# Kernel tuning notes

Measured on AMD Instinct MI355X. Metric: run time of the kernel, lower is better.

Reference implementation:

```python
import jax, jax.numpy as jnp
import numpy as np

B, T, D, H, L, V, CTX = 4, 2048, 256, 8, 12, 256, 2048
HD = D // H


def _ln(x, w, b, eps=1e-5):
    m = x.mean(-1, keepdims=True)
    v = ((x - m) ** 2).mean(-1, keepdims=True)
    return (x - m) * jax.lax.rsqrt(v + eps) * w + b


def setup_inputs() -> dict:
    key = jax.random.key(0)
    ks = jax.random.split(key, 16)
    s = 0.02
    inp = {
        "x": jax.random.randint(ks[0], (B, T), 0, V, dtype=jnp.int32),
        "tok_embed": jax.random.normal(ks[1], (V, D), jnp.float32) * s,
        "pos_embed": jax.random.normal(ks[2], (CTX, D), jnp.float32) * s,
        # stacked per-layer params (leading axis = layer)
        "ln1_w": jnp.ones((L, D), jnp.float32),
        "ln1_b": jnp.zeros((L, D), jnp.float32),
        "qkv_w": jax.random.normal(ks[3], (L, D, 3 * D), jnp.float32) * s,
        "qkv_b": jnp.zeros((L, 3 * D), jnp.float32),
        "out_w": jax.random.normal(ks[4], (L, D, D), jnp.float32) * s,
        "out_b": jnp.zeros((L, D), jnp.float32),
        "ln2_w": jnp.ones((L, D), jnp.float32),
        "ln2_b": jnp.zeros((L, D), jnp.float32),
        "fc1_w": jax.random.normal(ks[5], (L, D, 4 * D), jnp.float32) * s,
        "fc1_b": jnp.zeros((L, 4 * D), jnp.float32),
        "fc2_w": jax.random.normal(ks[6], (L, 4 * D, D), jnp.float32) * s,
        "fc2_b": jnp.zeros((L, D), jnp.float32),
        "lnf_w": jnp.ones((D,), jnp.float32),
        "lnf_b": jnp.zeros((D,), jnp.float32),
        "head_w": jax.random.normal(ks[7], (D, V), jnp.float32) * s,
        "head_b": jnp.zeros((V,), jnp.float32),
    }
    return inp


def _forward(x, tok_embed, pos_embed, ln1_w, ln1_b, qkv_w, qkv_b, out_w, out_b,
             ln2_w, ln2_b, fc1_w, fc1_b, fc2_w, fc2_b, lnf_w, lnf_b, head_w, head_b):
    Tcur = x.shape[1]
    h = tok_embed[x] + pos_embed[:Tcur][None, :, :]  # (B,T,D)
    causal = jnp.triu(jnp.ones((Tcur, Tcur), bool), k=1)  # True above diagonal
    scale = jnp.sqrt(jnp.asarray(HD, h.dtype))

    def step(h, p):
        (l1w, l1b, qw, qb, ow, ob, l2w, l2b, f1w, f1b, f2w, f2b) = p
        # attention
        z = _ln(h, l1w, l1b)
        qkv = z @ qw + qb  # (B,T,3D)
        qkv = qkv.reshape(h.shape[0], Tcur, 3, H, HD)
        q, k, v = qkv[:, :, 0], qkv[:, :, 1], qkv[:, :, 2]  # (B,T,H,HD)
        attn = jnp.einsum('bqhd,bkhd->bhqk', q, k) / scale
        attn = jnp.where(causal, -jnp.inf, attn)
        attn = jax.nn.softmax(attn, axis=-1)
        o = jnp.einsum('bhqk,bkhd->bqhd', attn, v).reshape(h.shape[0], Tcur, D)
        h = h + o @ ow + ob
        # MLP (torch nn.GELU default = exact erf gelu)
        z = _ln(h, l2w, l2b)
        z = jax.nn.gelu(z @ f1w + f1b, approximate=False)
        h = h + z @ f2w + f2b
        return h, None

    params = (ln1_w, ln1_b, qkv_w, qkv_b, out_w, out_b,
              ln2_w, ln2_b, fc1_w, fc1_b, fc2_w, fc2_b)
    h, _ = jax.lax.scan(step, h, params)
    h = _ln(h, lnf_w, lnf_b)
    return h @ head_w + head_b  # (B,T,V)


def reference(x, tok_embed, pos_embed, ln1_w, ln1_b, qkv_w, qkv_b, out_w, out_b,
              ln2_w, ln2_b, fc1_w, fc1_b, fc2_w, fc2_b, lnf_w, lnf_b, head_w, head_b):
    return _forward(x, tok_embed, pos_embed, ln1_w, ln1_b, qkv_w, qkv_b, out_w, out_b,
                    ln2_w, ln2_b, fc1_w, fc1_b, fc2_w, fc2_b, lnf_w, lnf_b, head_w, head_b)
```

## Files before the change

### kernel.cpp

```cpp
#include <hip/hip_runtime.h>
#include <cstdint>

#define TT 2048
#define DD 256
#define HH 8
#define LL 12

typedef __attribute__((ext_vector_type(8))) short s16x8;
typedef __attribute__((ext_vector_type(4))) float f32x4;

__device__ __forceinline__ unsigned short f2bf(float f) {
  union { float f; unsigned u; } v; v.f = f;
  return (unsigned short)((v.u + 0x7FFFu + ((v.u >> 16) & 1u)) >> 16);
}

__device__ __forceinline__ unsigned cvtpk(float lo, float hi) {
  unsigned r;
  asm("v_cvt_pk_bf16_f32 %0, %1, %2" : "=v"(r) : "v"(lo), "v"(hi));
  return r;
}

__device__ __forceinline__ float geluf(float x) {
  return 0.5f * x * (1.0f + erff(x * 0.70710678118654752f));
}

__device__ __forceinline__ float fexp2(float x) {
  float r;
  asm("v_exp_f32 %0, %1" : "=v"(r) : "v"(x));
  return r;
}

__device__ __forceinline__ void gload16(const void* g, void* l) {
  __builtin_amdgcn_global_load_lds((const __attribute__((address_space(1))) unsigned int*)g,
                                   (__attribute__((address_space(3))) unsigned int*)l, 16, 0, 0);
}

__global__ __launch_bounds__(256) void k_embed(const int* __restrict__ x,
                                               const float* __restrict__ tok,
                                               const float* __restrict__ pos,
                                               float* __restrict__ h) {
  int i = blockIdx.x * 256 + threadIdx.x;
  int row = i >> 6, c = i & 63;
  int t = x[row];
  f32x4 tv = ((const f32x4*)(tok + (size_t)t * DD))[c];
  f32x4 pv = ((const f32x4*)(pos + (size_t)(row & (TT - 1)) * DD))[c];
  ((f32x4*)(h + (size_t)row * DD))[c] = tv + pv;
}

__global__ __launch_bounds__(256) void k_ln(const float* __restrict__ h,
                                            const float* __restrict__ wgt,
                                            const float* __restrict__ bia,
                                            unsigned short* __restrict__ z) {
  int row = blockIdx.x * 4 + (threadIdx.x >> 6);
  int lane = threadIdx.x & 63;
  f32x4 v = ((const f32x4*)(h + (size_t)row * DD))[lane];
  float s = v[0] + v[1] + v[2] + v[3];
#pragma unroll
  for (int m = 32; m; m >>= 1) s += __shfl_xor(s, m);
  float mean = s * (1.0f / DD);
  f32x4 d = v - mean;
  float s2 = d[0] * d[0] + d[1] * d[1] + d[2] * d[2] + d[3] * d[3];
#pragma unroll
  for (int m = 32; m; m >>= 1) s2 += __shfl_xor(s2, m);
  float inv = rsqrtf(s2 * (1.0f / DD) + 1e-5f);
  f32x4 wv = ((const f32x4*)wgt)[lane];
  f32x4 bv = ((const f32x4*)bia)[lane];
  float o0 = d[0] * inv * wv[0] + bv[0], o1 = d[1] * inv * wv[1] + bv[1];
  float o2 = d[2] * inv * wv[2] + bv[2], o3 = d[3] * inv * wv[3] + bv[3];
  unsigned long long u64 = (unsigned long long)cvtpk(o0, o1) |
                           ((unsigned long long)cvtpk(o2, o3) << 32);
  *(unsigned long long*)(z + (size_t)row * DD + lane * 4) = u64;
}

__global__ __launch_bounds__(256) void k_cast_all(const float* __restrict__ qw, const float* __restrict__ ow,
                                                  const float* __restrict__ f1, const float* __restrict__ f2,
                                                  unsigned short* __restrict__ dst) {
  __shared__ float Tt[32][33];
  const int l = blockIdx.y;
  const int t = blockIdx.x;
  const float* src;
  unsigned short* d;
  int K, N, tk, tn;
  if (t < 192) {
    src = qw + (size_t)l * 196608; d = dst + (size_t)l * 786432;
    K = 256; N = 768; tk = t / 24; tn = t % 24;
  } else if (t < 256) {
    int t2 = t - 192;
    src = ow + (size_t)l * 65536; d = dst + (size_t)l * 786432 + 196608;
    K = 256; N = 256; tk = t2 >> 3; tn = t2 & 7;
  } else if (t < 512) {
    int t3 = t - 256;
    src = f1 + (size_t)l * 262144; d = dst + (size_t)l * 786432 + 262144;
    K = 256; N = 1024; tk = t3 >> 5; tn = t3 & 31;
  } else {
    int t4 = t - 512;
    src = f2 + (size_t)l * 262144; d = dst + (size_t)l * 786432 + 524288;
    K = 1024; N = 256; tk = t4 >> 3; tn = t4 & 7;
  }
  const int tx = threadIdx.x & 31, ty = threadIdx.x >> 5;
#pragma unroll
  for (int r = 0; r < 4; ++r) {
    int row = ty + r * 8;
    Tt[row][tx] = src[(size_t)(tk * 32 + row) * N + tn * 32 + tx];
  }
  __syncthreads();
#pragma unroll
  for (int r = 0; r < 4; ++r) {
    int row = ty + r * 8;
    d[(size_t)(tn * 32 + row) * K + tk * 32 + tx] = f2bf(Tt[tx][row]);
  }
}

__global__ __launch_bounds__(256) void k_cast_tr4(const float* __restrict__ qw, const float* __restrict__ ow,
                                                  const float* __restrict__ f1, const float* __restrict__ f2,
                                                  unsigned short* __restrict__ dq, unsigned short* __restrict__ dO,
                                                  unsigned short* __restrict__ d1, unsigned short* __restrict__ d2) {
// ... 66 lines not shown
      for (int ni = 0; ni < 4; ++ni)
        bf[ni] = *(const s16x8*)(Bs[buf] + (wc * 64 + ni * 16 + l15) * 64 + ks * 32 + g * 8);
#pragma unroll
      for (int mi = 0; mi < MI; ++mi)
#pragma unroll
        for (int ni = 0; ni < 4; ++ni)
          acc[mi][ni] = __builtin_amdgcn_mfma_f32_16x16x32_bf16(af[mi], bf[ni], acc[mi][ni], 0, 0, 0);
    }
    if (have_next) {
      __syncthreads();
      buf ^= 1;
    }
  }
#pragma unroll
  for (int ni = 0; ni < 4; ++ni) {
    int col = tn * 128 + wc * 64 + ni * 16 + l15;
    float bv = bias[col];
#pragma unroll
    for (int mi = 0; mi < MI; ++mi) {
      int row0 = tm * BM + wr * MI * 16 + mi * 16 + g * 4;
#pragma unroll
      for (int r = 0; r < 4; ++r) {
        size_t idx = (size_t)(row0 + r) * N + col;
        float vvv = acc[mi][ni][r] + bv;
        if (MODE == 0) ((unsigned short*)out)[idx] = f2bf(vvv);
        else if (MODE == 1) ((unsigned short*)out)[idx] = f2bf(geluf(vvv));
        else ((float*)out)[idx] = vvv;
      }
    }
  }
}

template <int NK>
__global__ __launch_bounds__(256, 2) void k_gemm_ln(const unsigned short* __restrict__ A,
                                                    const unsigned short* __restrict__ BT,
                                                    const float* __restrict__ bias,
                                                    float* __restrict__ h,
                                                    const float* __restrict__ lnw,
                                                    const float* __restrict__ lnb,
                                                    unsigned short* __restrict__ z) {
  __shared__ __align__(16) unsigned short As[2][32 * 64];
  __shared__ __align__(16) unsigned short Bs[2][256 * 64];
  const int tid = threadIdx.x;
  const int lane = tid & 63, wc = tid >> 6;
  const int l15 = lane & 15, g = lane >> 4;
  const int tm = blockIdx.x;
  const int K = NK * 64;
  f32x4 acc[2][4] = {};
  const unsigned short* Ag0 = A + (size_t)tm * 32 * K;

  gload16(Ag0 + (size_t)(tid >> 3) * K + (tid & 7) * 8, As[0] + tid * 8);
#pragma unroll
  for (int it = 0; it < 8; ++it) {
    int c = it * 256 + tid;
    gload16(BT + (size_t)(c >> 3) * K + (c & 7) * 8, Bs[0] + c * 8);
  }
  __syncthreads();

  int buf = 0;
  for (int kt = 0; kt < NK; ++kt) {
    const bool have_next = (kt + 1 < NK);
    if (have_next) {
      gload16(Ag0 + (size_t)(tid >> 3) * K + (kt + 1) * 64 + (tid & 7) * 8, As[buf ^ 1] + tid * 8);
#pragma unroll
      for (int it = 0; it < 8; ++it) {
        int c = it * 256 + tid;
        gload16(BT + (size_t)(c >> 3) * K + (kt + 1) * 64 + (c & 7) * 8, Bs[buf ^ 1] + c * 8);
      }
    }
#pragma unroll
    for (int ks = 0; ks < 2; ++ks) {
      s16x8 af[2], bf[4];
#pragma unroll
      for (int mi = 0; mi < 2; ++mi)
        af[mi] = *(const s16x8*)(As[buf] + (mi * 16 + l15) * 64 + ks * 32 + g * 8);
#pragma unroll
      for (int ni = 0; ni < 4; ++ni)
        bf[ni] = *(const s16x8*)(Bs[buf] + (wc * 64 + ni * 16 + l15) * 64 + ks * 32 + g * 8);
#pragma unroll
      for (int mi = 0; mi < 2; ++mi)
#pragma unroll
        for (int ni = 0; ni < 4; ++ni)
          acc[mi][ni] = __builtin_amdgcn_mfma_f32_16x16x32_bf16(af[mi], bf[ni], acc[mi][ni], 0, 0, 0);
    }
    if (have_next) {
      __syncthreads();
      buf ^= 1;
    }
  }
  const int row0 = tm * 32;
  float hv[2][4][4];
  float psum[2][4] = {}, psq[2][4] = {};
#pragma unroll
  for (int mi = 0; mi < 2; ++mi)
#pragma unroll
    for (int ni = 0; ni < 4; ++ni) {
      int col = wc * 64 + ni * 16 + l15;
      float bv = bias[col];
#pragma unroll
      for (int r = 0; r < 4; ++r) {
        int row = row0 + mi * 16 + g * 4 + r;
        float v = acc[mi][ni][r] + bv + h[(size_t)row * DD + col];
        hv[mi][ni][r] = v;
        h[(size_t)row * DD + col] = v;
        psum[mi][r] += v;
        psq[mi][r] += v * v;
      }
    }
#pragma unroll
  for (int m = 1; m < 16; m <<= 1)
#pragma unroll
    for (int mi = 0; mi < 2; ++mi)
#pragma unroll
      for (int r = 0; r < 4; ++r) {
        psum[mi][r] += __shfl_xor(psum[mi][r], m);
        psq[mi][r] += __shfl_xor(psq[mi][r], m);
      }
  __syncthreads();
  float* red = (float*)&As[0][0];
  if (l15 == 0) {
#pragma unroll
    for (int mi = 0; mi < 2; ++mi)
#pragma unroll
      for (int r = 0; r < 4; ++r) {
        int rw = mi * 16 + g * 4 + r;
        red[wc * 32 + rw] = psum[mi][r];
        red[128 + wc * 32 + rw] = psq[mi][r];
      }
  }
  __syncthreads();
  float mean[2][4], inv[2][4];
#pragma unroll
  for (int mi = 0; mi < 2; ++mi)
#pragma unroll
    for (int r = 0; r < 4; ++r) {
      int rw = mi * 16 + g * 4 + r;
      float s = (red[rw] + red[32 + rw]) + (red[64 + rw] + red[96 + rw]);
      float q = (red[128 + rw] + red[160 + rw]) + (red[192 + rw] + red[224 + rw]);
      float mn = s * (1.0f / DD);
      mean[mi][r] = mn;
      inv[mi][r] = rsqrtf(q * (1.0f / DD) - mn * mn + 1e-5f);
    }
#pragma unroll
  for (int ni = 0; ni < 4; ++ni) {
    int col = wc * 64 + ni * 16 + l15;
    float wv = lnw[col], bv = lnb[col];
#pragma unroll
    for (int mi = 0; mi < 2; ++mi)
#pragma unroll
      for (int r = 0; r < 4; ++r) {
        int row = row0 + mi * 16 + g * 4 + r;
        z[(size_t)row * DD + col] = f2bf((hv[mi][ni][r] - mean[mi][r]) * inv[mi][r] * wv + bv);
      }
  }
}

__global__ __launch_bounds__(512, 4) void k_attn(const unsigned short* __restrict__ qkv,
                                                 unsigned short* __restrict__ o) {
  __shared__ __align__(16) unsigned short Ks[2][128 * 40];
  __shared__ __align__(16) unsigned short Vs[2][2 * 32 * 72];
  const int tid = threadIdx.x, lane = tid & 63, wvi = tid >> 6;
  const int w = wvi >> 1, kh = wvi & 1;
  const int l15 = lane & 15, g = lane >> 4;
  const int p = blockIdx.x;
  const int b = blockIdx.y >> 3, hh = blockIdx.y & 7;
  const size_t base = (size_t)b * TT * 768 + hh * 32;
  const float scl2 = 0.25503492f;
  const int qt0 = p, qt1 = 31 - p;
  const int nt0 = (qt0 >> 1) + 1;
  const int krow = (wvi & 3) * 32 + (lane >> 1);
  const int khK = lane & 1;
  const int iv = wvi & 3;
  const int khv = iv >> 1, dh = iv & 1;

  s16x8 qf0 = *(const s16x8*)(qkv + base + (size_t)(qt0 * 64 + w * 16 + l15) * 768 + g * 8);
  s16x8 qf1 = *(const s16x8*)(qkv + base + (size_t)(qt1 * 64 + w * 16 + l15) * 768 + g * 8);

  if (wvi < 4) {
    const unsigned short* kp = qkv + base + (size_t)krow * 768 + 256 + khK * 16;
    s16x8 k0 = *(const s16x8*)kp;
    s16x8 k1 = *(const s16x8*)(kp + 8);
    *(s16x8*)(Ks[0] + krow * 40 + khK * 16) = k0;
    *(s16x8*)(Ks[0] + krow * 40 + khK * 16 + 8) = k1;
  } else {
    const unsigned short* vp = qkv + base + (size_t)(khv * 64 + lane) * 768 + 512 + dh * 16;
    s16x8 v0 = *(const s16x8*)vp;
    s16x8 v1 = *(const s16x8*)(vp + 8);
    unsigned short* vb = Vs[0] + khv * 2304;
#pragma unroll
    for (int e = 0; e < 8; ++e) {
      int d0 = dh * 16 + e, d1 = dh * 16 + 8 + e;
      vb[d0 * 72 + (lane ^ (((d0 >> 3) & 3) << 4))] = (unsigned short)v0[e];
      vb[d1 * 72 + (lane ^ (((d1 >> 3) & 3) << 4))] = (unsigned short)v1[e];
    }
  }
  __syncthreads();

  f32x4 accO[2] = {};
  float mM = -3.0e38f, ls = 0.f;

  for (int t = 0; t < 17; ++t) {
    const int buf = t & 1;
    const bool ph = (t >= nt0);
    const int qt = ph ? qt1 : qt0;
    const int j = ph ? t - nt0 : t;
    const bool have_next = (t + 1 < 17);
    unsigned short* ps = (wvi < 4) ? (Ks[buf ^ 1] + wvi * 1280)
                                   : (Vs[buf ^ 1] + (wvi - 4) * 1152);
    s16x8 k0n, k1n, v0n, v1n;
    if (have_next) {
      const int jn = (t + 1 >= nt0) ? t + 1 - nt0 : t + 1;
      if (wvi < 4) {
        const unsigned short* kp = qkv + base + (size_t)(jn * 128 + krow) * 768 + 256 + khK * 16;
        k0n = *(const s16x8*)kp;
        k1n = *(const s16x8*)(kp + 8);
      } else {
        const unsigned short* vp = qkv + base + (size_t)(jn * 128 + khv * 64 + lane) * 768 + 512 + dh * 16;
        v0n = *(const s16x8*)vp;
        v1n = *(const s16x8*)(vp + 8);
      }
    }
    const int rel = qt * 64 + w * 16 - j * 128;
    int cbg = (rel + 15) >> 4; if (cbg > 7) cbg = 7;
    const int cbm = (cbg - kh * 4 > 3) ? 3 : cbg - kh * 4;
    if (cbm >= 0) {
      const bool fullw = (rel >= kh * 64 + 63);
      f32x4 st[4];
#pragma unroll
      for (int c = 0; c < 4; ++c)
        if (c <= cbm) {
          s16x8 kf = *(const s16x8*)(Ks[buf] + (kh * 64 + c * 16 + l15) * 40 + g * 8);
          f32x4 zz = {};
          st[c] = __builtin_amdgcn_mfma_f32_16x16x32_bf16(kf, ph ? qf1 : qf0, zz, 0, 0, 0);
        }
      float rmax = -3.0e38f;
#pragma unroll
      for (int c = 0; c < 4; ++c)
        if (c <= cbm) {
          if (!fullw) {
#pragma unroll
            for (int r = 0; r < 4; ++r)
              if ((kh * 64 + c * 16 + g * 4 + r) > rel + l15) st[c][r] = -3.0e38f;
          }
#pragma unroll
          for (int r = 0; r < 4; ++r) rmax = fmaxf(rmax, st[c][r]);
        }
      rmax = fmaxf(rmax, __shfl_xor(rmax, 16));
      rmax = fmaxf(rmax, __shfl_xor(rmax, 32));
      const float rs = rmax * scl2;
      float al = 1.0f;
      if (!__all(rs <= mM + 11.5f)) {
        float nm = fmaxf(mM, rs);
        al = fexp2(mM - nm);
        mM = nm;
#pragma unroll
        for (int r = 0; r < 4; ++r) {
          float aw = __shfl(al, g * 4 + r);
          accO[0][r] *= aw;
          accO[1][r] *= aw;
        }
      }
      float rsum = 0.f;
#pragma unroll
      for (int c = 0; c < 4; ++c)
        if (c <= cbm) {
          float e0 = fexp2(fmaf(st[c][0], scl2, -mM));
          float e1 = fexp2(fmaf(st[c][1], scl2, -mM));
          float e2 = fexp2(fmaf(st[c][2], scl2, -mM));
          float e3 = fexp2(fmaf(st[c][3], scl2, -mM));
          rsum += (e0 + e1) + (e2 + e3);
          unsigned long long u = (unsigned long long)cvtpk(e0, e1) |
                                 ((unsigned long long)cvtpk(e2, e3) << 32);
          *(unsigned long long*)(ps + l15 * 72 + c * 16 + g * 4) = u;
        }
      if (cbm < 3 && !(cbm & 1))
        *(unsigned long long*)(ps + l15 * 72 + (cbm + 1) * 16 + g * 4) = 0ULL;
      rsum += __shfl_xor(rsum, 16);
      rsum += __shfl_xor(rsum, 32);
      ls = ls * al + rsum;
      asm volatile("s_waitcnt lgkmcnt(0)" ::: "memory");
      __builtin_amdgcn_sched_barrier(0);
      const int kcm = cbm >> 1;
#pragma unroll
      for (int kc = 0; kc < 2; ++kc)
        if (kc <= kcm) {
          s16x8 pa = *(const s16x8*)(ps + l15 * 72 + kc * 32 + g * 8);
          s16x8 bv0, bv1;
#pragma unroll
          for (int hb = 0; hb < 2; ++hb) {
            const int d = hb * 16 + l15;
            const int kx = (kc * 32 + g * 8) ^ (((d >> 3) & 3) << 4);
            if (hb == 0) bv0 = *(const s16x8*)(Vs[buf] + kh * 2304 + d * 72 + kx);
            else bv1 = *(const s16x8*)(Vs[buf] + kh * 2304 + d * 72 + kx);
          }
          accO[0] = __builtin_amdgcn_mfma_f32_16x16x32_bf16(pa, bv0, accO[0], 0, 0, 0);
          accO[1] = __builtin_amdgcn_mfma_f32_16x16x32_bf16(pa, bv1, accO[1], 0, 0, 0);
        }
    }
    if (have_next) {
      if (wvi < 4) {
        *(s16x8*)(Ks[buf ^ 1] + krow * 40 + khK * 16) = k0n;
        *(s16x8*)(Ks[buf ^ 1] + krow * 40 + khK * 16 + 8) = k1n;
      } else {
        unsigned short* vb = Vs[buf ^ 1] + khv * 2304;
#pragma unroll
        for (int e = 0; e < 8; ++e) {
          int d0 = dh * 16 + e, d1 = dh * 16 + 8 + e;
          vb[d0 * 72 + (lane ^ (((d0 >> 3) & 3) << 4))] = (unsigned short)v0n[e];
          vb[d1 * 72 + (lane ^ (((d1 >> 3) & 3) << 4))] = (unsigned short)v1n[e];
        }
      }
      __syncthreads();
    }
    if (t == nt0 - 1) {
      float* sc = (float*)((wvi < 4) ? (Ks[buf] + wvi * 1280) : (Vs[buf] + (wvi - 4) * 1152));
#pragma unroll
      for (int hb = 0; hb < 2; ++hb)
#pragma unroll
        for (int r = 0; r < 4; ++r) sc[(g * 4 + r) * 32 + hb * 16 + l15] = accO[hb][r];
      if (g == 0) { sc[512 + l15] = mM; sc[528 + l15] = ls; }
      __syncthreads();
      if (kh == 0) {
        const int pw = wvi + 1;
        float* pb = (float*)((pw < 4) ? (Ks[buf] + pw * 1280) : (Vs[buf] + (pw - 4) * 1152));
#pragma unroll
        for (int r = 0; r < 4; ++r) {
          int q = g * 4 + r;
          float mA = __shfl(mM, q), lA = __shfl(ls, q);
          float mB = pb[512 + q], lB = pb[528 + q];
          float M = fmaxf(mA, mB);
          float eA = fexp2(mA - M), eB = fexp2(mB - M);
          float inv = 1.0f / (eA * lA + eB * lB);
          int row = qt0 * 64 + w * 16 + q;
#pragma unroll
          for (int hb = 0; hb < 2; ++hb) {
            float ob = pb[q * 32 + hb * 16 + l15];
            float val = (eA * accO[hb][r] + eB * ob) * inv;
            o[(size_t)(b * TT + row) * DD + hh * 32 + hb * 16 + l15] = f2bf(val);
          }
        }
      }
      __syncthreads();
      accO[0] = f32x4{};
      accO[1] = f32x4{};
      mM = -3.0e38f;
      ls = 0.f;
    }
  }
  {
    __syncthreads();
    float* sc = (float*)((wvi < 4) ? (Ks[0] + wvi * 1280) : (Vs[0] + (wvi - 4) * 1152));
#pragma unroll
    for (int hb = 0; hb < 2; ++hb)
#pragma unroll
      for (int r = 0; r < 4; ++r) sc[(g * 4 + r) * 32 + hb * 16 + l15] = accO[hb][r];
    if (g == 0) { sc[512 + l15] = mM; sc[528 + l15] = ls; }
    __syncthreads();
    if (kh == 0) {
      const int pw = wvi + 1;
      float* pb = (float*)((pw < 4) ? (Ks[0] + pw * 1280) : (Vs[0] + (pw - 4) * 1152));
#pragma unroll
      for (int r = 0; r < 4; ++r) {
        int q = g * 4 + r;
        float mA = __shfl(mM, q), lA = __shfl(ls, q);
        float mB = pb[512 + q], lB = pb[528 + q];
        float M = fmaxf(mA, mB);
        float eA = fexp2(mA - M), eB = fexp2(mB - M);
        float inv = 1.0f / (eA * lA + eB * lB);
        int row = qt1 * 64 + w * 16 + q;
#pragma unroll
        for (int hb = 0; hb < 2; ++hb) {
          float ob = pb[q * 32 + hb * 16 + l15];
          float val = (eA * accO[hb][r] + eB * ob) * inv;
          o[(size_t)(b * TT + row) * DD + hh * 32 + hb * 16 + l15] = f2bf(val);
        }
      }
    }
  }
}

extern "C" void kernel_launch(void* const* d_in, const int* in_sizes, int n_in,
                              void* d_out, int out_size, void* d_ws, size_t ws_size,
                              hipStream_t stream) {
  const int* x = (const int*)d_in[0];
  const float* tok = (const float*)d_in[1];
  const float* pos = (const float*)d_in[2];
  const float* ln1w = (const float*)d_in[3];
  const float* ln1b = (const float*)d_in[4];
  const float* qkvw = (const float*)d_in[5];
  const float* qkvb = (const float*)d_in[6];
  const float* outw = (const float*)d_in[7];
  const float* outb = (const float*)d_in[8];
  const float* ln2w = (const float*)d_in[9];
  const float* ln2b = (const float*)d_in[10];
  const float* f1w = (const float*)d_in[11];
  const float* f1b = (const float*)d_in[12];
  const float* f2w = (const float*)d_in[13];
  const float* f2b = (const float*)d_in[14];
  const float* lnfw = (const float*)d_in[15];
  const float* lnfb = (const float*)d_in[16];
  const float* hw = (const float*)d_in[17];
  const float* hb = (const float*)d_in[18];

  char* ws = (char*)d_ws;
  float* h = (float*)(ws + 0);
  unsigned short* z = (unsigned short*)(ws + 8388608);
  unsigned short* qkvB = (unsigned short*)(ws + 12582912);
  unsigned short* ob = (unsigned short*)(ws + 25165824);
  unsigned short* a1 = (unsigned short*)(ws + 29360128);
  unsigned short* wAll = (unsigned short*)(ws + 46137344);
  const bool bigws = ws_size >= 65142784ULL;
  unsigned short* wh = (unsigned short*)(ws + (bigws ? 65011712 : 47710208));

  if (bigws)
    k_cast_all<<<dim3(768, 12), dim3(256), 0, stream>>>(qkvw, outw, f1w, f2w, wAll);
  k_cast_tr256<<<dim3(256), dim3(256), 0, stream>>>(hw, wh);
  k_embed<<<dim3(2048), dim3(256), 0, stream>>>(x, tok, pos, h);
  k_ln<<<dim3(2048), dim3(256), 0, stream>>>(h, ln1w, ln1b, z);

  for (int l = 0; l < LL; ++l) {
    unsigned short* wq = wAll + (size_t)(bigws ? l : 0) * 786432;
    unsigned short* wo = wq + 196608;
    unsigned short* w1 = wo + 65536;
    unsigned short* w2 = w1 + 262144;
    if (!bigws)
      k_cast_tr4<<<dim3(1024), dim3(256), 0, stream>>>(
          qkvw + (size_t)l * 196608, outw + (size_t)l * 65536,
          f1w + (size_t)l * 262144, f2w + (size_t)l * 262144, wq, wo, w1, w2);
    k_gemm<0, 2><<<dim3(6, 128), dim3(256), 0, stream>>>(z, wq, qkvb + l * 768, qkvB, nullptr, 8192, 768, 256);
    k_attn<<<dim3(16, 32), dim3(512), 0, stream>>>(qkvB, ob);
    k_gemm_ln<4><<<dim3(256), dim3(256), 0, stream>>>(ob, wo, outb + l * 256, h,
                                                      ln2w + l * 256, ln2b + l * 256, z);
    k_gemm<1, 2><<<dim3(8, 128), dim3(256), 0, stream>>>(z, w1, f1b + l * 1024, a1, nullptr, 8192, 1024, 256);
    const float* nw = (l == LL - 1) ? lnfw : ln1w + (l + 1) * 256;
    const float* nb = (l == LL - 1) ? lnfb : ln1b + (l + 1) * 256;
    k_gemm_ln<16><<<dim3(256), dim3(256), 0, stream>>>(a1, w2, f2b + l * 256, h, nw, nb, z);
  }

  k_gemm<3, 2><<<dim3(2, 128), dim3(256), 0, stream>>>(z, wh, hb, d_out, nullptr, 8192, 256, 256);
}
```

Before: 1.288 ms.

## Split attention key tile four ways across waves and halve query tile size

The attention kernel now uses 32-row query tiles, paired as p and 63-p, and launches twice as many blocks. Each wave handles a 16-query slice against a quarter (32 keys) of each 128-key tile instead of a half. The four partial softmax states are merged at the end through shared memory, and launch bounds are raised to target more resident blocks. The aim is more parallelism and shorter per-wave dependency chains, paid for with extra merge work, more redundant K/V tile loads per query, and more register pressure.

```diff
diff --git a/kernel.cpp b/kernel.cpp
--- a/kernel.cpp
+++ b/kernel.cpp
@@ -337,26 +337,26 @@
   }
 }
 
-__global__ __launch_bounds__(512, 4) void k_attn(const unsigned short* __restrict__ qkv,
+__global__ __launch_bounds__(512, 8) void k_attn(const unsigned short* __restrict__ qkv,
                                                  unsigned short* __restrict__ o) {
   __shared__ __align__(16) unsigned short Ks[2][128 * 40];
   __shared__ __align__(16) unsigned short Vs[2][2 * 32 * 72];
   const int tid = threadIdx.x, lane = tid & 63, wvi = tid >> 6;
-  const int w = wvi >> 1, kh = wvi & 1;
+  const int w = wvi >> 2, kq = wvi & 3;
   const int l15 = lane & 15, g = lane >> 4;
   const int p = blockIdx.x;
   const int b = blockIdx.y >> 3, hh = blockIdx.y & 7;
   const size_t base = (size_t)b * TT * 768 + hh * 32;
   const float scl2 = 0.25503492f;
-  const int qt0 = p, qt1 = 31 - p;
-  const int nt0 = (qt0 >> 1) + 1;
+  const int qt0 = p, qt1 = 63 - p;
+  const int nt0 = (qt0 >> 2) + 1;
   const int krow = (wvi & 3) * 32 + (lane >> 1);
   const int khK = lane & 1;
   const int iv = wvi & 3;
   const int khv = iv >> 1, dh = iv & 1;
 
-  s16x8 qf0 = *(const s16x8*)(qkv + base + (size_t)(qt0 * 64 + w * 16 + l15) * 768 + g * 8);
-  s16x8 qf1 = *(const s16x8*)(qkv + base + (size_t)(qt1 * 64 + w * 16 + l15) * 768 + g * 8);
+  s16x8 qf0 = *(const s16x8*)(qkv + base + (size_t)(qt0 * 32 + w * 16 + l15) * 768 + g * 8);
+  s16x8 qf1 = *(const s16x8*)(qkv + base + (size_t)(qt1 * 32 + w * 16 + l15) * 768 + g * 8);
 
   if (wvi < 4) {
     const unsigned short* kp = qkv + base + (size_t)krow * 768 + 256 + khK * 16;
@@ -402,27 +402,27 @@
         v1n = *(const s16x8*)(vp + 8);
       }
     }
-    const int rel = qt * 64 + w * 16 - j * 128;
+    const int rel = qt * 32 + w * 16 - j * 128;
     int cbg = (rel + 15) >> 4; if (cbg > 7) cbg = 7;
-    const int cbm = (cbg - kh * 4 > 3) ? 3 : cbg - kh * 4;
+    const int cbm = (cbg - kq * 2 > 1) ? 1 : cbg - kq * 2;
     if (cbm >= 0) {
-      const bool fullw = (rel >= kh * 64 + 63);
-      f32x4 st[4];
-#pragma unroll
-      for (int c = 0; c < 4; ++c)
+      const bool fullw = (rel >= kq * 32 + 31);
+      f32x4 st[2];
+#pragma unroll
+      for (int c = 0; c < 2; ++c)
         if (c <= cbm) {
-          s16x8 kf = *(const s16x8*)(Ks[buf] + (kh * 64 + c * 16 + l15) * 40 + g * 8);
+          s16x8 kf = *(const s16x8*)(Ks[buf] + (kq * 32 + c * 16 + l15) * 40 + g * 8);
           f32x4 zz = {};
           st[c] = __builtin_amdgcn_mfma_f32_16x16x32_bf16(kf, ph ? qf1 : qf0, zz, 0, 0, 0);
         }
       float rmax = -3.0e38f;
 #pragma unroll
-      for (int c = 0; c < 4; ++c)
+      for (int c = 0; c < 2; ++c)
         if (c <= cbm) {
           if (!fullw) {
 #pragma unroll
             for (int r = 0; r < 4; ++r)
-              if ((kh * 64 + c * 16 + g * 4 + r) > rel + l15) st[c][r] = -3.0e38f;
+              if ((kq * 32 + c * 16 + g * 4 + r) > rel + l15) st[c][r] = -3.0e38f;
           }
 #pragma unroll
           for (int r = 0; r < 4; ++r) rmax = fmaxf(rmax, st[c][r]);
@@ -444,7 +444,7 @@
       }
       float rsum = 0.f;
 #pragma unroll
-      for (int c = 0; c < 4; ++c)
+      for (int c = 0; c < 2; ++c)
         if (c <= cbm) {
           float e0 = fexp2(fmaf(st[c][0], scl2, -mM));
           float e1 = fexp2(fmaf(st[c][1], scl2, -mM));
@@ -453,31 +453,28 @@
           rsum += (e0 + e1) + (e2 + e3);
           unsigned long long u = (unsigned long long)cvtpk(e0, e1) |
                                  ((unsigned long long)cvtpk(e2, e3) << 32);
-          *(unsigned long long*)(ps + l15 * 72 + c * 16 + g * 4) = u;
-        }
-      if (cbm < 3 && !(cbm & 1))
-        *(unsigned long long*)(ps + l15 * 72 + (cbm + 1) * 16 + g * 4) = 0ULL;
+          *(unsigned long long*)(ps + l15 * 40 + c * 16 + g * 4) = u;
+        }
+      if (cbm < 1)
+        *(unsigned long long*)(ps + l15 * 40 + 16 + g * 4) = 0ULL;
       rsum += __shfl_xor(rsum, 16);
       rsum += __shfl_xor(rsum, 32);
       ls = ls * al + rsum;
       asm volatile("s_waitcnt lgkmcnt(0)" ::: "memory");
       __builtin_amdgcn_sched_barrier(0);
-      const int kcm = cbm >> 1;
-#pragma unroll
-      for (int kc = 0; kc < 2; ++kc)
-        if (kc <= kcm) {
-          s16x8 pa = *(const s16x8*)(ps + l15 * 72 + kc * 32 + g * 8);
-          s16x8 bv0, bv1;
-#pragma unroll
-          for (int hb = 0; hb < 2; ++hb) {
-            const int d = hb * 16 + l15;
-            const int kx = (kc * 32 + g * 8) ^ (((d >> 3) & 3) << 4);
-            if (hb == 0) bv0 = *(const s16x8*)(Vs[buf] + kh * 2304 + d * 72 + kx);
-            else bv1 = *(const s16x8*)(Vs[buf] + kh * 2304 + d * 72 + kx);
-          }
-          accO[0] = __builtin_amdgcn_mfma_f32_16x16x32_bf16(pa, bv0, accO[0], 0, 0, 0);
-          accO[1] = __builtin_amdgcn_mfma_f32_16x16x32_bf16(pa, bv1, accO[1], 0, 0, 0);
-        }
+      {
+        s16x8 pa = *(const s16x8*)(ps + l15 * 40 + g * 8);
+        s16x8 bv0, bv1;
+#pragma unroll
+        for (int hb = 0; hb < 2; ++hb) {
+          const int d = hb * 16 + l15;
+          const int kx = ((kq & 1) * 32 + g * 8) ^ (((d >> 3) & 3) << 4);
+          if (hb == 0) bv0 = *(const s16x8*)(Vs[buf] + (kq >> 1) * 2304 + d * 72 + kx);
+          else bv1 = *(const s16x8*)(Vs[buf] + (kq >> 1) * 2304 + d * 72 + kx);
+        }
+        accO[0] = __builtin_amdgcn_mfma_f32_16x16x32_bf16(pa, bv0, accO[0], 0, 0, 0);
+        accO[1] = __builtin_amdgcn_mfma_f32_16x16x32_bf16(pa, bv1, accO[1], 0, 0, 0);
+      }
     }
     if (have_next) {
       if (wvi < 4) {
@@ -502,23 +499,26 @@
         for (int r = 0; r < 4; ++r) sc[(g * 4 + r) * 32 + hb * 16 + l15] = accO[hb][r];
       if (g == 0) { sc[512 + l15] = mM; sc[528 + l15] = ls; }
       __syncthreads();
-      if (kh == 0) {
-        const int pw = wvi + 1;
-        float* pb = (float*)((pw < 4) ? (Ks[buf] + pw * 1280) : (Vs[buf] + (pw - 4) * 1152));
+      if (kq == 0) {
+        const float* pb1 = (const float*)((wvi + 1 < 4) ? (Ks[buf] + (wvi + 1) * 1280) : (Vs[buf] + (wvi - 3) * 1152));
+        const float* pb2 = (const float*)((wvi + 2 < 4) ? (Ks[buf] + (wvi + 2) * 1280) : (Vs[buf] + (wvi - 2) * 1152));
+        const float* pb3 = (const float*)((wvi + 3 < 4) ? (Ks[buf] + (wvi + 3) * 1280) : (Vs[buf] + (wvi - 1) * 1152));
 #pragma unroll
         for (int r = 0; r < 4; ++r) {
           int q = g * 4 + r;
-          float mA = __shfl(mM, q), lA = __shfl(ls, q);
-          float mB = pb[512 + q], lB = pb[528 + q];
-          float M = fmaxf(mA, mB);
-          float eA = fexp2(mA - M), eB = fexp2(mB - M);
-          float inv = 1.0f / (eA * lA + eB * lB);
-          int row = qt0 * 64 + w * 16 + q;
+          float m0 = __shfl(mM, q), l0 = __shfl(ls, q);
+          float m1 = pb1[512 + q], l1 = pb1[528 + q];
+          float m2 = pb2[512 + q], l2 = pb2[528 + q];
+          float m3 = pb3[512 + q], l3 = pb3[528 + q];
+          float M = fmaxf(fmaxf(m0, m1), fmaxf(m2, m3));
+          float e0 = fexp2(m0 - M), e1 = fexp2(m1 - M), e2 = fexp2(m2 - M), e3 = fexp2(m3 - M);
+          float inv = 1.0f / (e0 * l0 + e1 * l1 + e2 * l2 + e3 * l3);
+          int row = qt0 * 32 + w * 16 + q;
 #pragma unroll
           for (int hb = 0; hb < 2; ++hb) {
-            float ob = pb[q * 32 + hb * 16 + l15];
-            float val = (eA * accO[hb][r] + eB * ob) * inv;
-            o[(size_t)(b * TT + row) * DD + hh * 32 + hb * 16 + l15] = f2bf(val);
+            int oi = q * 32 + hb * 16 + l15;
+            float val = e0 * accO[hb][r] + e1 * pb1[oi] + e2 * pb2[oi] + e3 * pb3[oi];
+            o[(size_t)(b * TT + row) * DD + hh * 32 + hb * 16 + l15] = f2bf(val * inv);
           }
         }
       }
@@ -538,23 +538,26 @@
       for (int r = 0; r < 4; ++r) sc[(g * 4 + r) * 32 + hb * 16 + l15] = accO[hb][r];
     if (g == 0) { sc[512 + l15] = mM; sc[528 + l15] = ls; }
     __syncthreads();
-    if (kh == 0) {
-      const int pw = wvi + 1;
-      float* pb = (float*)((pw < 4) ? (Ks[0] + pw * 1280) : (Vs[0] + (pw - 4) * 1152));
+    if (kq == 0) {
+      const float* pb1 = (const float*)((wvi + 1 < 4) ? (Ks[0] + (wvi + 1) * 1280) : (Vs[0] + (wvi - 3) * 1152));
+      const float* pb2 = (const float*)((wvi + 2 < 4) ? (Ks[0] + (wvi + 2) * 1280) : (Vs[0] + (wvi - 2) * 1152));
+      const float* pb3 = (const float*)((wvi + 3 < 4) ? (Ks[0] + (wvi + 3) * 1280) : (Vs[0] + (wvi - 1) * 1152));
 #pragma unroll
       for (int r = 0; r < 4; ++r) {
         int q = g * 4 + r;
-        float mA = __shfl(mM, q), lA = __shfl(ls, q);
-        float mB = pb[512 + q], lB = pb[528 + q];
-        float M = fmaxf(mA, mB);
-        float eA = fexp2(mA - M), eB = fexp2(mB - M);
-        float inv = 1.0f / (eA * lA + eB * lB);
-        int row = qt1 * 64 + w * 16 + q;
+        float m0 = __shfl(mM, q), l0 = __shfl(ls, q);
+        float m1 = pb1[512 + q], l1 = pb1[528 + q];
+        float m2 = pb2[512 + q], l2 = pb2[528 + q];
+        float m3 = pb3[512 + q], l3 = pb3[528 + q];
+        float M = fmaxf(fmaxf(m0, m1), fmaxf(m2, m3));
+        float e0 = fexp2(m0 - M), e1 = fexp2(m1 - M), e2 = fexp2(m2 - M), e3 = fexp2(m3 - M);
+        float inv = 1.0f / (e0 * l0 + e1 * l1 + e2 * l2 + e3 * l3);
+        int row = qt1 * 32 + w * 16 + q;
 #pragma unroll
         for (int hb = 0; hb < 2; ++hb) {
-          float ob = pb[q * 32 + hb * 16 + l15];
-          float val = (eA * accO[hb][r] + eB * ob) * inv;
-          o[(size_t)(b * TT + row) * DD + hh * 32 + hb * 16 + l15] = f2bf(val);
+          int oi = q * 32 + hb * 16 + l15;
+          float val = e0 * accO[hb][r] + e1 * pb1[oi] + e2 * pb2[oi] + e3 * pb3[oi];
+          o[(size_t)(b * TT + row) * DD + hh * 32 + hb * 16 + l15] = f2bf(val * inv);
         }
       }
     }
@@ -610,7 +613,7 @@
           qkvw + (size_t)l * 196608, outw + (size_t)l * 65536,
           f1w + (size_t)l * 262144, f2w + (size_t)l * 262144, wq, wo, w1, w2);
     k_gemm<0, 2><<<dim3(6, 128), dim3(256), 0, stream>>>(z, wq, qkvb + l * 768, qkvB, nullptr, 8192, 768, 256);
-    k_attn<<<dim3(16, 32), dim3(512), 0, stream>>>(qkvB, ob);
+    k_attn<<<dim3(32, 32), dim3(512), 0, stream>>>(qkvB, ob);
     k_gemm_ln<4><<<dim3(256), dim3(256), 0, stream>>>(ob, wo, outb + l * 256, h,
                                                       ln2w + l * 256, ln2b + l * 256, z);
     k_gemm<1, 2><<<dim3(8, 128), dim3(256), 0, stream>>>(z, w1, f1b + l * 1024, a1, nullptr, 8192, 1024, 256);
```

Result: slower. 4.135 ms (+221.2%).

## Fuse embed with first layernorm, fold head cast, widen gemm_ln to 8 waves

Applied to the files above, without the earlier changes.

Merges the embedding gather and the first layernorm into one kernel and folds the head-weight cast into the batched weight-cast launch, removing launches and an extra pass over h. The fused GEMM+residual+layernorm kernel now uses 512 threads, so each of 8 waves computes 32 output columns. The residual read is prefetched before the K loop. This is meant to raise occupancy and latency hiding for the 256-block grid, at the cost of a larger cross-wave reduction and a shared reduction buffer that must be twice as large.

```diff
diff --git a/kernel.cpp b/kernel.cpp
--- a/kernel.cpp
+++ b/kernel.cpp
@@ -35,25 +35,20 @@
                                    (__attribute__((address_space(3))) unsigned int*)l, 16, 0, 0);
 }
 
-__global__ __launch_bounds__(256) void k_embed(const int* __restrict__ x,
-                                               const float* __restrict__ tok,
-                                               const float* __restrict__ pos,
-                                               float* __restrict__ h) {
-  int i = blockIdx.x * 256 + threadIdx.x;
-  int row = i >> 6, c = i & 63;
-  int t = x[row];
-  f32x4 tv = ((const f32x4*)(tok + (size_t)t * DD))[c];
-  f32x4 pv = ((const f32x4*)(pos + (size_t)(row & (TT - 1)) * DD))[c];
-  ((f32x4*)(h + (size_t)row * DD))[c] = tv + pv;
-}
-
-__global__ __launch_bounds__(256) void k_ln(const float* __restrict__ h,
-                                            const float* __restrict__ wgt,
-                                            const float* __restrict__ bia,
-                                            unsigned short* __restrict__ z) {
+__global__ __launch_bounds__(256) void k_embed_ln(const int* __restrict__ x,
+                                                  const float* __restrict__ tok,
+                                                  const float* __restrict__ pos,
+                                                  const float* __restrict__ wgt,
+                                                  const float* __restrict__ bia,
+                                                  float* __restrict__ h,
+                                                  unsigned short* __restrict__ z) {
   int row = blockIdx.x * 4 + (threadIdx.x >> 6);
   int lane = threadIdx.x & 63;
-  f32x4 v = ((const f32x4*)(h + (size_t)row * DD))[lane];
+  int t = x[row];
+  f32x4 tv = ((const f32x4*)(tok + (size_t)t * DD))[lane];
+  f32x4 pv = ((const f32x4*)(pos + (size_t)(row & (TT - 1)) * DD))[lane];
+  f32x4 v = tv + pv;
+  ((f32x4*)(h + (size_t)row * DD))[lane] = v;
   float s = v[0] + v[1] + v[2] + v[3];
 #pragma unroll
   for (int m = 32; m; m >>= 1) s += __shfl_xor(s, m);
@@ -74,6 +69,7 @@
 
 __global__ __launch_bounds__(256) void k_cast_all(const float* __restrict__ qw, const float* __restrict__ ow,
                                                   const float* __restrict__ f1, const float* __restrict__ f2,
+                                                  const float* __restrict__ hw,
                                                   unsigned short* __restrict__ dst) {
   __shared__ float Tt[32][33];
   const int l = blockIdx.y;
@@ -81,7 +77,11 @@
   const float* src;
   unsigned short* d;
   int K, N, tk, tn;
-  if (t < 192) {
+  if (l == 12) {
+    if (t >= 64) return;
+    src = hw; d = dst + (size_t)12 * 786432;
+    K = 256; N = 256; tk = t >> 3; tn = t & 7;
+  } else if (t < 192) {
     src = qw + (size_t)l * 196608; d = dst + (size_t)l * 786432;
     K = 256; N = 768; tk = t / 24; tn = t % 24;
   } else if (t < 256) {
@@ -214,7 +214,7 @@
 }
 
 template <int NK>
-__global__ __launch_bounds__(256, 2) void k_gemm_ln(const unsigned short* __restrict__ A,
+__global__ __launch_bounds__(512, 2) void k_gemm_ln(const unsigned short* __restrict__ A,
                                                     const unsigned short* __restrict__ BT,
                                                     const float* __restrict__ bias,
                                                     float* __restrict__ h,
@@ -228,13 +228,25 @@
   const int l15 = lane & 15, g = lane >> 4;
   const int tm = blockIdx.x;
   const int K = NK * 64;
-  f32x4 acc[2][4] = {};
+  const int row0 = tm * 32;
+  f32x4 acc[2][2] = {};
   const unsigned short* Ag0 = A + (size_t)tm * 32 * K;
 
-  gload16(Ag0 + (size_t)(tid >> 3) * K + (tid & 7) * 8, As[0] + tid * 8);
-#pragma unroll
-  for (int it = 0; it < 8; ++it) {
-    int c = it * 256 + tid;
+  float rv[2][2][4];
+#pragma unroll
+  for (int mi = 0; mi < 2; ++mi)
+#pragma unroll
+    for (int ni = 0; ni < 2; ++ni) {
+      int col = wc * 32 + ni * 16 + l15;
+#pragma unroll
+      for (int r = 0; r < 4; ++r)
+        rv[mi][ni][r] = h[(size_t)(row0 + mi * 16 + g * 4 + r) * DD + col];
+    }
+
+  if (tid < 256) gload16(Ag0 + (size_t)(tid >> 3) * K + (tid & 7) * 8, As[0] + tid * 8);
+#pragma unroll
+  for (int it = 0; it < 4; ++it) {
+    int c = it * 512 + tid;
     gload16(BT + (size_t)(c >> 3) * K + (c & 7) * 8, Bs[0] + c * 8);
   }
   __syncthreads();
@@ -243,26 +255,27 @@
   for (int kt = 0; kt < NK; ++kt) {
     const bool have_next = (kt + 1 < NK);
     if (have_next) {
-      gload16(Ag0 + (size_t)(tid >> 3) * K + (kt + 1) * 64 + (tid & 7) * 8, As[buf ^ 1] + tid * 8);
-#pragma unroll
-      for (int it = 0; it < 8; ++it) {
-        int c = it * 256 + tid;
+      if (tid < 256)
+        gload16(Ag0 + (size_t)(tid >> 3) * K + (kt + 1) * 64 + (tid & 7) * 8, As[buf ^ 1] + tid * 8);
+#pragma unroll
+      for (int it = 0; it < 4; ++it) {
+        int c = it * 512 + tid;
         gload16(BT + (size_t)(c >> 3) * K + (kt + 1) * 64 + (c & 7) * 8, Bs[buf ^ 1] + c * 8);
       }
     }
 #pragma unroll
     for (int ks = 0; ks < 2; ++ks) {
-      s16x8 af[2], bf[4];
+      s16x8 af[2], bf[2];
 #pragma unroll
       for (int mi = 0; mi < 2; ++mi)
         af[mi] = *(const s16x8*)(As[buf] + (mi * 16 + l15) * 64 + ks * 32 + g * 8);
 #pragma unroll
-      for (int ni = 0; ni < 4; ++ni)
-        bf[ni] = *(const s16x8*)(Bs[buf] + (wc * 64 + ni * 16 + l15) * 64 + ks * 32 + g * 8);
+      for (int ni = 0; ni < 2; ++ni)
+        bf[ni] = *(const s16x8*)(Bs[buf] + (wc * 32 + ni * 16 + l15) * 64 + ks * 32 + g * 8);
 #pragma unroll
       for (int mi = 0; mi < 2; ++mi)
 #pragma unroll
-        for (int ni = 0; ni < 4; ++ni)
+        for (int ni = 0; ni < 2; ++ni)
           acc[mi][ni] = __builtin_amdgcn_mfma_f32_16x16x32_bf16(af[mi], bf[ni], acc[mi][ni], 0, 0, 0);
     }
     if (have_next) {
@@ -270,19 +283,18 @@
       buf ^= 1;
     }
   }
-  const int row0 = tm * 32;
-  float hv[2][4][4];
+  float hv[2][2][4];
   float psum[2][4] = {}, psq[2][4] = {};
 #pragma unroll
   for (int mi = 0; mi < 2; ++mi)
 #pragma unroll
-    for (int ni = 0; ni < 4; ++ni) {
-      int col = wc * 64 + ni * 16 + l15;
+    for (int ni = 0; ni < 2; ++ni) {
+      int col = wc * 32 + ni * 16 + l15;
       float bv = bias[col];
 #pragma unroll
       for (int r = 0; r < 4; ++r) {
         int row = row0 + mi * 16 + g * 4 + r;
-        float v = acc[mi][ni][r] + bv + h[(size_t)row * DD + col];
+        float v = acc[mi][ni][r] + bv + rv[mi][ni][r];
         hv[mi][ni][r] = v;
         h[(size_t)row * DD + col] = v;
         psum[mi][r] += v;
@@ -307,7 +319,7 @@
       for (int r = 0; r < 4; ++r) {
         int rw = mi * 16 + g * 4 + r;
         red[wc * 32 + rw] = psum[mi][r];
-        red[128 + wc * 32 + rw] = psq[mi][r];
+        red[256 + wc * 32 + rw] = psq[mi][r];
       }
   }
   __syncthreads();
@@ -317,22 +329,26 @@
 #pragma unroll
     for (int r = 0; r < 4; ++r) {
       int rw = mi * 16 + g * 4 + r;
-      float s = (red[rw] + red[32 + rw]) + (red[64 + rw] + red[96 + rw]);
-      float q = (red[128 + rw] + red[160 + rw]) + (red[192 + rw] + red[224 + rw]);
+      float s = 0.f, q = 0.f;
+#pragma unroll
+      for (int wv = 0; wv < 8; ++wv) {
+        s += red[wv * 32 + rw];
+        q += red[256 + wv * 32 + rw];
+      }
       float mn = s * (1.0f / DD);
       mean[mi][r] = mn;
       inv[mi][r] = rsqrtf(q * (1.0f / DD) - mn * mn + 1e-5f);
     }
 #pragma unroll
-  for (int ni = 0; ni < 4; ++ni) {
-    int col = wc * 64 + ni * 16 + l15;
-    float wv = lnw[col], bv = lnb[col];
+  for (int ni = 0; ni < 2; ++ni) {
+    int col = wc * 32 + ni * 16 + l15;
+    float wvv = lnw[col], bvv = lnb[col];
 #pragma unroll
     for (int mi = 0; mi < 2; ++mi)
 #pragma unroll
       for (int r = 0; r < 4; ++r) {
         int row = row0 + mi * 16 + g * 4 + r;
-        z[(size_t)row * DD + col] = f2bf((hv[mi][ni][r] - mean[mi][r]) * inv[mi][r] * wv + bv);
+        z[(size_t)row * DD + col] = f2bf((hv[mi][ni][r] - mean[mi][r]) * inv[mi][r] * wvv + bvv);
       }
   }
 }
@@ -595,10 +611,10 @@
   unsigned short* wh = (unsigned short*)(ws + (bigws ? 65011712 : 47710208));
 
   if (bigws)
-    k_cast_all<<<dim3(768, 12), dim3(256), 0, stream>>>(qkvw, outw, f1w, f2w, wAll);
-  k_cast_tr256<<<dim3(256), dim3(256), 0, stream>>>(hw, wh);
-  k_embed<<<dim3(2048), dim3(256), 0, stream>>>(x, tok, pos, h);
-  k_ln<<<dim3(2048), dim3(256), 0, stream>>>(h, ln1w, ln1b, z);
+    k_cast_all<<<dim3(768, 13), dim3(256), 0, stream>>>(qkvw, outw, f1w, f2w, hw, wAll);
+  else
+    k_cast_tr256<<<dim3(256), dim3(256), 0, stream>>>(hw, wh);
+  k_embed_ln<<<dim3(2048), dim3(256), 0, stream>>>(x, tok, pos, ln1w, ln1b, h, z);
 
   for (int l = 0; l < LL; ++l) {
     unsigned short* wq = wAll + (size_t)(bigws ? l : 0) * 786432;
@@ -611,12 +627,12 @@
           f1w + (size_t)l * 262144, f2w + (size_t)l * 262144, wq, wo, w1, w2);
     k_gemm<0, 2><<<dim3(6, 128), dim3(256), 0, stream>>>(z, wq, qkvb + l * 768, qkvB, nullptr, 8192, 768, 256);
     k_attn<<<dim3(16, 32), dim3(512), 0, stream>>>(qkvB, ob);
-    k_gemm_ln<4><<<dim3(256), dim3(256), 0, stream>>>(ob, wo, outb + l * 256, h,
+    k_gemm_ln<4><<<dim3(256), dim3(512), 0, stream>>>(ob, wo, outb + l * 256, h,
                                                       ln2w + l * 256, ln2b + l * 256, z);
     k_gemm<1, 2><<<dim3(8, 128), dim3(256), 0, stream>>>(z, w1, f1b + l * 1024, a1, nullptr, 8192, 1024, 256);
     const float* nw = (l == LL - 1) ? lnfw : ln1w + (l + 1) * 256;
     const float* nb = (l == LL - 1) ? lnfb : ln1b + (l + 1) * 256;
-    k_gemm_ln<16><<<dim3(256), dim3(256), 0, stream>>>(a1, w2, f2b + l * 256, h, nw, nb, z);
+    k_gemm_ln<16><<<dim3(256), dim3(512), 0, stream>>>(a1, w2, f2b + l * 256, h, nw, nb, z);
   }
 
   k_gemm<3, 2><<<dim3(2, 128), dim3(256), 0, stream>>>(z, wh, hb, d_out, nullptr, 8192, 256, 256);
```

Result: no change. 1.292 ms (+0.4%).

## Double attention key tile to 256 rows and have all waves load K and V

Applied to the files above, without the earlier changes.

Raises the attention key/value tile from 128 to 256 keys, which halves the loop trips (9 instead of 17) and the number of block-wide barriers per tile pair. All 512 threads now load both K and V, instead of splitting waves between them. A barrier is added before the next-tile shared-memory stores so the P scratch aliasing the other buffer stays safe. The cost is roughly doubled LDS per block, which may limit occupancy, plus more wasted masked work on diagonal tiles.

```diff
diff --git a/kernel.cpp b/kernel.cpp
--- a/kernel.cpp
+++ b/kernel.cpp
@@ -339,8 +339,8 @@
 
 __global__ __launch_bounds__(512, 4) void k_attn(const unsigned short* __restrict__ qkv,
                                                  unsigned short* __restrict__ o) {
-  __shared__ __align__(16) unsigned short Ks[2][128 * 40];
-  __shared__ __align__(16) unsigned short Vs[2][2 * 32 * 72];
+  __shared__ __align__(16) unsigned short Ks[2][256 * 40];
+  __shared__ __align__(16) unsigned short Vs[2][2 * 32 * 136];
   const int tid = threadIdx.x, lane = tid & 63, wvi = tid >> 6;
   const int w = wvi >> 1, kh = wvi & 1;
   const int l15 = lane & 15, g = lane >> 4;
@@ -349,31 +349,29 @@
   const size_t base = (size_t)b * TT * 768 + hh * 32;
   const float scl2 = 0.25503492f;
   const int qt0 = p, qt1 = 31 - p;
-  const int nt0 = (qt0 >> 1) + 1;
-  const int krow = (wvi & 3) * 32 + (lane >> 1);
-  const int khK = lane & 1;
-  const int iv = wvi & 3;
-  const int khv = iv >> 1, dh = iv & 1;
+  const int nt0 = (qt0 >> 2) + 1;
+  const int krow = tid >> 1, khK = tid & 1;
+  const int vk = tid & 255, vdh = tid >> 8;
+  const int vkh = vk >> 7, vklo = vk & 127;
 
   s16x8 qf0 = *(const s16x8*)(qkv + base + (size_t)(qt0 * 64 + w * 16 + l15) * 768 + g * 8);
   s16x8 qf1 = *(const s16x8*)(qkv + base + (size_t)(qt1 * 64 + w * 16 + l15) * 768 + g * 8);
 
-  if (wvi < 4) {
+  {
     const unsigned short* kp = qkv + base + (size_t)krow * 768 + 256 + khK * 16;
     s16x8 k0 = *(const s16x8*)kp;
     s16x8 k1 = *(const s16x8*)(kp + 8);
     *(s16x8*)(Ks[0] + krow * 40 + khK * 16) = k0;
     *(s16x8*)(Ks[0] + krow * 40 + khK * 16 + 8) = k1;
-  } else {
-    const unsigned short* vp = qkv + base + (size_t)(khv * 64 + lane) * 768 + 512 + dh * 16;
+    const unsigned short* vp = qkv + base + (size_t)vk * 768 + 512 + vdh * 16;
     s16x8 v0 = *(const s16x8*)vp;
     s16x8 v1 = *(const s16x8*)(vp + 8);
-    unsigned short* vb = Vs[0] + khv * 2304;
+    unsigned short* vb = Vs[0] + vkh * 4352;
 #pragma unroll
     for (int e = 0; e < 8; ++e) {
-      int d0 = dh * 16 + e, d1 = dh * 16 + 8 + e;
-      vb[d0 * 72 + (lane ^ (((d0 >> 3) & 3) << 4))] = (unsigned short)v0[e];
-      vb[d1 * 72 + (lane ^ (((d1 >> 3) & 3) << 4))] = (unsigned short)v1[e];
+      int d0 = vdh * 16 + e, d1 = vdh * 16 + 8 + e;
+      vb[d0 * 136 + (vklo ^ (((d0 >> 3) & 3) << 4))] = (unsigned short)v0[e];
+      vb[d1 * 136 + (vklo ^ (((d1 >> 3) & 3) << 4))] = (unsigned short)v1[e];
     }
   }
   __syncthreads();
@@ -381,48 +379,45 @@
   f32x4 accO[2] = {};
   float mM = -3.0e38f, ls = 0.f;
 
-  for (int t = 0; t < 17; ++t) {
+  for (int t = 0; t < 9; ++t) {
     const int buf = t & 1;
     const bool ph = (t >= nt0);
     const int qt = ph ? qt1 : qt0;
     const int j = ph ? t - nt0 : t;
-    const bool have_next = (t + 1 < 17);
-    unsigned short* ps = (wvi < 4) ? (Ks[buf ^ 1] + wvi * 1280)
-                                   : (Vs[buf ^ 1] + (wvi - 4) * 1152);
+    const bool have_next = (t + 1 < 9);
+    unsigned short* ps = (wvi < 4) ? (Ks[buf ^ 1] + wvi * 2560)
+                                   : (Vs[buf ^ 1] + (wvi - 4) * 2176);
     s16x8 k0n, k1n, v0n, v1n;
     if (have_next) {
       const int jn = (t + 1 >= nt0) ? t + 1 - nt0 : t + 1;
-      if (wvi < 4) {
-        const unsigned short* kp = qkv + base + (size_t)(jn * 128 + krow) * 768 + 256 + khK * 16;
-        k0n = *(const s16x8*)kp;
-        k1n = *(const s16x8*)(kp + 8);
-      } else {
-        const unsigned short* vp = qkv + base + (size_t)(jn * 128 + khv * 64 + lane) * 768 + 512 + dh * 16;
-        v0n = *(const s16x8*)vp;
-        v1n = *(const s16x8*)(vp + 8);
-      }
-    }
-    const int rel = qt * 64 + w * 16 - j * 128;
-    int cbg = (rel + 15) >> 4; if (cbg > 7) cbg = 7;
-    const int cbm = (cbg - kh * 4 > 3) ? 3 : cbg - kh * 4;
+      const unsigned short* kp = qkv + base + (size_t)(jn * 256 + krow) * 768 + 256 + khK * 16;
+      k0n = *(const s16x8*)kp;
+      k1n = *(const s16x8*)(kp + 8);
+      const unsigned short* vp = qkv + base + (size_t)(jn * 256 + vk) * 768 + 512 + vdh * 16;
+      v0n = *(const s16x8*)vp;
+      v1n = *(const s16x8*)(vp + 8);
+    }
+    const int rel = qt * 64 + w * 16 - j * 256;
+    int cbg = (rel + 15) >> 4; if (cbg > 15) cbg = 15;
+    const int cbm = (cbg - kh * 8 > 7) ? 7 : cbg - kh * 8;
     if (cbm >= 0) {
-      const bool fullw = (rel >= kh * 64 + 63);
-      f32x4 st[4];
-#pragma unroll
-      for (int c = 0; c < 4; ++c)
+      const bool fullw = (rel >= kh * 128 + 127);
+      f32x4 st[8];
+#pragma unroll
+      for (int c = 0; c < 8; ++c)
         if (c <= cbm) {
-          s16x8 kf = *(const s16x8*)(Ks[buf] + (kh * 64 + c * 16 + l15) * 40 + g * 8);
+          s16x8 kf = *(const s16x8*)(Ks[buf] + (kh * 128 + c * 16 + l15) * 40 + g * 8);
           f32x4 zz = {};
           st[c] = __builtin_amdgcn_mfma_f32_16x16x32_bf16(kf, ph ? qf1 : qf0, zz, 0, 0, 0);
         }
       float rmax = -3.0e38f;
 #pragma unroll
-      for (int c = 0; c < 4; ++c)
+      for (int c = 0; c < 8; ++c)
         if (c <= cbm) {
           if (!fullw) {
 #pragma unroll
             for (int r = 0; r < 4; ++r)
-              if ((kh * 64 + c * 16 + g * 4 + r) > rel + l15) st[c][r] = -3.0e38f;
+              if ((kh * 128 + c * 16 + g * 4 + r) > rel + l15) st[c][r] = -3.0e38f;
           }
 #pragma unroll
           for (int r = 0; r < 4; ++r) rmax = fmaxf(rmax, st[c][r]);
@@ -444,7 +439,7 @@
       }
       float rsum = 0.f;
 #pragma unroll
-      for (int c = 0; c < 4; ++c)
+      for (int c = 0; c < 8; ++c)
         if (c <= cbm) {
           float e0 = fexp2(fmaf(st[c][0], scl2, -mM));
           float e1 = fexp2(fmaf(st[c][1], scl2, -mM));
@@ -453,10 +448,10 @@
           rsum += (e0 + e1) + (e2 + e3);
           unsigned long long u = (unsigned long long)cvtpk(e0, e1) |
                                  ((unsigned long long)cvtpk(e2, e3) << 32);
-          *(unsigned long long*)(ps + l15 * 72 + c * 16 + g * 4) = u;
+          *(unsigned long long*)(ps + l15 * 136 + c * 16 + g * 4) = u;
         }
-      if (cbm < 3 && !(cbm & 1))
-        *(unsigned long long*)(ps + l15 * 72 + (cbm + 1) * 16 + g * 4) = 0ULL;
+      if (cbm < 7 && !(cbm & 1))
+        *(unsigned long long*)(ps + l15 * 136 + (cbm + 1) * 16 + g * 4) = 0ULL;
       rsum += __shfl_xor(rsum, 16);
       rsum += __shfl_xor(rsum, 32);
       ls = ls * al + rsum;
@@ -464,38 +459,36 @@
       __builtin_amdgcn_sched_barrier(0);
       const int kcm = cbm >> 1;
 #pragma unroll
-      for (int kc = 0; kc < 2; ++kc)
+      for (int kc = 0; kc < 4; ++kc)
         if (kc <= kcm) {
-          s16x8 pa = *(const s16x8*)(ps + l15 * 72 + kc * 32 + g * 8);
+          s16x8 pa = *(const s16x8*)(ps + l15 * 136 + kc * 32 + g * 8);
           s16x8 bv0, bv1;
 #pragma unroll
           for (int hb = 0; hb < 2; ++hb) {
             const int d = hb * 16 + l15;
             const int kx = (kc * 32 + g * 8) ^ (((d >> 3) & 3) << 4);
-            if (hb == 0) bv0 = *(const s16x8*)(Vs[buf] + kh * 2304 + d * 72 + kx);
-            else bv1 = *(const s16x8*)(Vs[buf] + kh * 2304 + d * 72 + kx);
+            if (hb == 0) bv0 = *(const s16x8*)(Vs[buf] + kh * 4352 + d * 136 + kx);
+            else bv1 = *(const s16x8*)(Vs[buf] + kh * 4352 + d * 136 + kx);
           }
           accO[0] = __builtin_amdgcn_mfma_f32_16x16x32_bf16(pa, bv0, accO[0], 0, 0, 0);
           accO[1] = __builtin_amdgcn_mfma_f32_16x16x32_bf16(pa, bv1, accO[1], 0, 0, 0);
         }
     }
     if (have_next) {
-      if (wvi < 4) {
-        *(s16x8*)(Ks[buf ^ 1] + krow * 40 + khK * 16) = k0n;
-        *(s16x8*)(Ks[buf ^ 1] + krow * 40 + khK * 16 + 8) = k1n;
-      } else {
-        unsigned short* vb = Vs[buf ^ 1] + khv * 2304;
-#pragma unroll
-        for (int e = 0; e < 8; ++e) {
-          int d0 = dh * 16 + e, d1 = dh * 16 + 8 + e;
-          vb[d0 * 72 + (lane ^ (((d0 >> 3) & 3) << 4))] = (unsigned short)v0n[e];
-          vb[d1 * 72 + (lane ^ (((d1 >> 3) & 3) << 4))] = (unsigned short)v1n[e];
-        }
-      }
       __syncthreads();
+      *(s16x8*)(Ks[buf ^ 1] + krow * 40 + khK * 16) = k0n;
+      *(s16x8*)(Ks[buf ^ 1] + krow * 40 + khK * 16 + 8) = k1n;
+      unsigned short* vb = Vs[buf ^ 1] + vkh * 4352;
+#pragma unroll
+      for (int e = 0; e < 8; ++e) {
+        int d0 = vdh * 16 + e, d1 = vdh * 16 + 8 + e;
+        vb[d0 * 136 + (vklo ^ (((d0 >> 3) & 3) << 4))] = (unsigned short)v0n[e];
+        vb[d1 * 136 + (vklo ^ (((d1 >> 3) & 3) << 4))] = (unsigned short)v1n[e];
+      }
+      __syncthreads();
     }
     if (t == nt0 - 1) {
-      float* sc = (float*)((wvi < 4) ? (Ks[buf] + wvi * 1280) : (Vs[buf] + (wvi - 4) * 1152));
+      float* sc = (float*)((wvi < 4) ? (Ks[buf] + wvi * 2560) : (Vs[buf] + (wvi - 4) * 2176));
 #pragma unroll
       for (int hb = 0; hb < 2; ++hb)
 #pragma unroll
@@ -504,7 +497,7 @@
       __syncthreads();
       if (kh == 0) {
         const int pw = wvi + 1;
-        float* pb = (float*)((pw < 4) ? (Ks[buf] + pw * 1280) : (Vs[buf] + (pw - 4) * 1152));
+        float* pb = (float*)((pw < 4) ? (Ks[buf] + pw * 2560) : (Vs[buf] + (pw - 4) * 2176));
 #pragma unroll
         for (int r = 0; r < 4; ++r) {
           int q = g * 4 + r;
@@ -531,7 +524,7 @@
   }
   {
     __syncthreads();
-    float* sc = (float*)((wvi < 4) ? (Ks[0] + wvi * 1280) : (Vs[0] + (wvi - 4) * 1152));
+    float* sc = (float*)((wvi < 4) ? (Ks[0] + wvi * 2560) : (Vs[0] + (wvi - 4) * 2176));
 #pragma unroll
     for (int hb = 0; hb < 2; ++hb)
 #pragma unroll
@@ -540,7 +533,7 @@
     __syncthreads();
     if (kh == 0) {
       const int pw = wvi + 1;
-      float* pb = (float*)((pw < 4) ? (Ks[0] + pw * 1280) : (Vs[0] + (pw - 4) * 1152));
+      float* pb = (float*)((pw < 4) ? (Ks[0] + pw * 2560) : (Vs[0] + (pw - 4) * 2176));
 #pragma unroll
       for (int r = 0; r < 4; ++r) {
         int q = g * 4 + r;
```

Result: slower. 1.608 ms (+24.9%).
